# Performance work log

Hardware: AMD Instinct MI355X
Metric: run time of the kernel (lower is better)

## Reference

```python
import jax, jax.numpy as jnp
import numpy as np

B, H, N, D = 4, 8, 4096, 64
M = 266  # nb_features = int(D * ln(D))
CHUNK = 128
KERNEL_EPS = 1e-4


def _gaussian_orthogonal_random_matrix(nb_rows, nb_cols, rng):
    # scaling == 0: rows are orthogonal blocks rescaled by norms of iid gaussian rows
    blocks = []
    n_full = nb_rows // nb_cols
    for _ in range(n_full):
        q, _ = np.linalg.qr(rng.standard_normal((nb_cols, nb_cols)))
        blocks.append(q.T)
    rem = nb_rows - n_full * nb_cols
    if rem > 0:
        q, _ = np.linalg.qr(rng.standard_normal((nb_cols, nb_cols)))
        blocks.append(q.T[:rem])
    final = np.concatenate(blocks, axis=0)
    multiplier = np.linalg.norm(rng.standard_normal((nb_rows, nb_cols)), axis=1)
    return (multiplier[:, None] * final).astype(np.float32)


def setup_inputs() -> dict:
    key = jax.random.key(0)
    kq, kk, kv = jax.random.split(key, 3)
    rng = np.random.default_rng(0)
    return {
        "q": jax.random.normal(kq, (B, H, N, D), dtype=jnp.float32),
        "k": jax.random.normal(kk, (B, H, N, D), dtype=jnp.float32),
        "v": jax.random.normal(kv, (B, H, N, D), dtype=jnp.float32),
        "projection_matrix": jnp.asarray(
            _gaussian_orthogonal_random_matrix(M, D, rng)),
    }


def _softmax_kernel(data, projection_matrix, is_query):
    # data: [b,h,n,d], projection: [m,d]
    d = data.shape[-1]
    data_normalizer = d ** (-0.25)
    ratio = projection_matrix.shape[0] ** (-0.5)
    data_dash = jnp.einsum('bhnd,md->bhnm', data_normalizer * data,
                           projection_matrix)
    diag_data = jnp.sum(data ** 2, axis=-1) * 0.5 * data_normalizer ** 2  # [b,h,n]
    if is_query:
        stab = jnp.max(data_dash, axis=-1, keepdims=True)
    else:
        stab = jnp.max(data_dash)  # global max, as in torch reference
    return ratio * (jnp.exp(data_dash - diag_data[..., None] - stab) + KERNEL_EPS)


def _causal_linear_attention(qp, kp, v, chunk=CHUNK):
    # qp,kp: [b,h,n,m]; v: [b,h,n,e]; chunked causal cumulative-sum scan
    b, h, n, m = qp.shape
    e = v.shape[-1]
    nc = n // chunk
    qc = qp.reshape(b, h, nc, chunk, m).transpose(2, 0, 1, 3, 4)
    kc = kp.reshape(b, h, nc, chunk, m).transpose(2, 0, 1, 3, 4)
    vc = v.reshape(b, h, nc, chunk, e).transpose(2, 0, 1, 3, 4)

    def step(carry, inp):
        k_sum, ctx_sum = carry  # [b,h,m], [b,h,m,e]
        qch, kch, vch = inp     # [b,h,c,m], [b,h,c,m], [b,h,c,e]
        k_cs = k_sum[:, :, None, :] + jnp.cumsum(kch, axis=2)  # [b,h,c,m]
        D_inv = 1.0 / jnp.einsum('bhcm,bhcm->bhc', qch, k_cs)
        ctx = ctx_sum[:, :, None] + jnp.cumsum(
            jnp.einsum('bhcm,bhce->bhcme', kch, vch), axis=2)  # [b,h,c,m,e]
        out = jnp.einsum('bhcme,bhcm,bhc->bhce', ctx, qch, D_inv)
        return (k_cs[:, :, -1], ctx[:, :, -1]), out

    init = (jnp.zeros((b, h, m), qp.dtype), jnp.zeros((b, h, m, e), qp.dtype))
    _, outs = jax.lax.scan(step, init, (qc, kc, vc))
    return outs.transpose(1, 2, 0, 3, 4).reshape(b, h, n, e)


def reference(q, k, v, projection_matrix):
    qp = _softmax_kernel(q, projection_matrix, is_query=True)
    kp = _softmax_kernel(k, projection_matrix, is_query=False)
    return _causal_linear_attention(qp, kp, v)
```

## Files before the change

### kernel.cpp

```cpp
#include <hip/hip_runtime.h>

#define BB 4
#define HH 8
#define NSEQ 4096
#define DD 64
#define MM 266
#define CCH 128
#define NCH 32
#define NBH (BB*HH)
#define NROWS (NBH*NSEQ)

#define NORMALIZER 0.35355339059327373f
#define DIAGF 0.0625f
#define RATIO 0.0613140017f
#define KEPS 1e-4f
#define SBIAS 4.0f

typedef unsigned short ushort_t;
typedef unsigned int uint_t;

typedef __attribute__((ext_vector_type(8))) short bf16x8;
typedef __attribute__((ext_vector_type(4))) float f32x4;

__device__ __forceinline__ f32x4 mfma16(bf16x8 a, bf16x8 b, f32x4 c){
  return __builtin_amdgcn_mfma_f32_16x16x32_bf16(a, b, c, 0, 0, 0);
}

__device__ __forceinline__ ushort_t f2bf(float x){
  union { float f; uint_t u; } v; v.f = x;
  uint_t r = (v.u + 0x7FFFu + ((v.u >> 16) & 1u)) >> 16;
  return (ushort_t)r;
}
__device__ __forceinline__ float bf2f(ushort_t h){
  union { uint_t u; float f; } v; v.u = ((uint_t)h) << 16;
  return v.f;
}
__device__ __forceinline__ void unpack2(uint_t w, float& lo, float& hi){
  union { uint_t u; float f; } a, b;
  a.u = w << 16; b.u = w & 0xFFFF0000u;
  lo = a.f; hi = b.f;
}

__device__ __forceinline__ uint_t fenc(float f){
  uint_t b = __float_as_uint(f);
  return (b & 0x80000000u) ? ~b : (b | 0x80000000u);
}
__device__ __forceinline__ float fdec(uint_t u){
  uint_t b = (u >> 31) ? (u ^ 0x80000000u) : ~u;
  return __uint_as_float(b);
}

__device__ __forceinline__ bf16x8 frag_ld(const ushort_t* tile, int stride, int s0, int koff){
  const int l = threadIdx.x & 63;
  return *(const bf16x8*)(tile + (s0 + (l&15))*stride + koff + ((l>>4)<<3));
}


__global__ __launch_bounds__(256) void k_dash_both(const float* __restrict__ q,
                                                   const float* __restrict__ k,
                                                   const float* __restrict__ proj,
                                                   ushort_t* __restrict__ qp,
                                                   ushort_t* __restrict__ kd,
                                                   uint_t* __restrict__ gmaxu){
  __shared__ __align__(16) ushort_t pjs[272*72];
  __shared__ __align__(16) ushort_t qs[128*72];
  __shared__ float diags[128];
  __shared__ float smax[4];
  const int t = threadIdx.x;
  const bool isq = blockIdx.x < (NROWS/128);
  const int blk = isq ? blockIdx.x : (blockIdx.x - NROWS/128);
  const float* x = isq ? q : k;

  #pragma unroll
  for (int h=0; h<2; ++h){
    float2 pv[17];
    #pragma unroll
    for (int i=0;i<17;++i){
      int idx = t + (h*17+i)*256;
      int m = idx>>5, dp = (idx&31)*2;
      float2 p2 = {0.f,0.f};
      if (m < MM) p2 = *(const float2*)(proj + (size_t)m*DD + dp);
      pv[i] = p2;
    }
    #pragma unroll
    for (int i=0;i<17;++i){
      int idx = t + (h*17+i)*256;
      int m = idx>>5, dp = (idx&31)*2;
      *(uint_t*)(pjs + m*72 + dp) = (uint_t)f2bf(pv[i].x) | ((uint_t)f2bf(pv[i].y)<<16);
    }
  }
  {
    const int row = t>>1, half = t&1;
    const float2* xr = (const float2*)(x + ((size_t)blk*128 + row)*DD + half*32);
    float ss = 0.f;
    #pragma unroll
    for (int i=0;i<16;++i){
      float2 a = xr[i];
      ss += a.x*a.x + a.y*a.y;
      uint_t w = (uint_t)f2bf(a.x*NORMALIZER) | ((uint_t)f2bf(a.y*NORMALIZER)<<16);
      *(uint_t*)(qs + row*72 + half*32 + i*2) = w;
    }
    ss += __shfl_xor(ss, 1);
    if (half==0) diags[row] = ss*DIAGF;
  }
  __syncthreads();

  const int l = t&63, wv = t>>6;
  const int wr0 = wv*32;
  float dv[2][4];
  #pragma unroll
  for (int rt=0;rt<2;++rt)
    #pragma unroll
    for (int r=0;r<4;++r) dv[rt][r] = diags[wr0 + rt*16 + ((l>>4)<<2) + r];

  const size_t growb = (size_t)blk*128;

  if (isq){
    float rmax[2][4];
    #pragma unroll
    for (int rt=0;rt<2;++rt){ rmax[rt][0]=-3e38f; rmax[rt][1]=-3e38f; rmax[rt][2]=-3e38f; rmax[rt][3]=-3e38f; }
    uint_t spu[17][2][2];
    #pragma unroll
    for (int mt=0; mt<17; ++mt){
      bf16x8 b0 = frag_ld(pjs, 72, mt*16, 0);
      bf16x8 b1 = frag_ld(pjs, 72, mt*16, 32);
      const bool valid = (mt*16 + (l&15)) < MM;
      #pragma unroll
      for (int rt=0;rt<2;++rt){
        bf16x8 a0 = frag_ld(qs, 72, wr0+rt*16, 0);
        bf16x8 a1 = frag_ld(qs, 72, wr0+rt*16, 32);
        f32x4 acc = {0.f,0.f,0.f,0.f};
        acc = mfma16(a0, b0, acc);
        acc = mfma16(a1, b1, acc);
        float sp0 = acc[0]-dv[rt][0]+SBIAS, sp1 = acc[1]-dv[rt][1]+SBIAS;
        float sp2 = acc[2]-dv[rt][2]+SBIAS, sp3 = acc[3]-dv[rt][3]+SBIAS;
        if (valid){
          rmax[rt][0] = fmaxf(rmax[rt][0], sp0); rmax[rt][1] = fmaxf(rmax[rt][1], sp1);
          rmax[rt][2] = fmaxf(rmax[rt][2], sp2); rmax[rt][3] = fmaxf(rmax[rt][3], sp3);
        }
        spu[mt][rt][0] = (uint_t)f2bf(sp0) | ((uint_t)f2bf(sp1)<<16);
        spu[mt][rt][1] = (uint_t)f2bf(sp2) | ((uint_t)f2bf(sp3)<<16);
      }
    }
    float sub[2][4];
    #pragma unroll
    for (int rt=0;rt<2;++rt){
      #pragma unroll
      for (int r=0;r<4;++r){
        float m = rmax[rt][r];
        m = fmaxf(m, __shfl_xor(m,1)); m = fmaxf(m, __shfl_xor(m,2));
        m = fmaxf(m, __shfl_xor(m,4)); m = fmaxf(m, __shfl_xor(m,8));
        sub[rt][r] = m + dv[rt][r];
      }
    }
    #pragma unroll
    for (int mt=0; mt<17; ++mt){
      const int m = mt*16 + (l&15);
      if (m < MM){
        #pragma unroll
        for (int rt=0;rt<2;++rt){
          float a0,a1,a2,a3;
          unpack2(spu[mt][rt][0], a0, a1);
          unpack2(spu[mt][rt][1], a2, a3);
          const size_t rb = growb + wr0 + rt*16 + ((l>>4)<<2);
          qp[(rb+0)*MM + m] = f2bf(RATIO*(__expf(a0 - sub[rt][0]) + KEPS));
          qp[(rb+1)*MM + m] = f2bf(RATIO*(__expf(a1 - sub[rt][1]) + KEPS));
          qp[(rb+2)*MM + m] = f2bf(RATIO*(__expf(a2 - sub[rt][2]) + KEPS));
          qp[(rb+3)*MM + m] = f2bf(RATIO*(__expf(a3 - sub[rt][3]) + KEPS));
        }
      }
    }
  } else {
    float rmax[2][4];
    #pragma unroll
    for (int rt=0;rt<2;++rt){ rmax[rt][0]=-3e38f; rmax[rt][1]=-3e38f; rmax[rt][2]=-3e38f; rmax[rt][3]=-3e38f; }
    for (int mt=0; mt<17; ++mt){
      bf16x8 b0 = frag_ld(pjs, 72, mt*16, 0);
      bf16x8 b1 = frag_ld(pjs, 72, mt*16, 32);
      const int m = mt*16 + (l&15);
      const bool valid = (m < MM);
      #pragma unroll
      for (int rt=0;rt<2;++rt){
        bf16x8 a0 = frag_ld(qs, 72, wr0+rt*16, 0);
        bf16x8 a1 = frag_ld(qs, 72, wr0+rt*16, 32);
        f32x4 acc = {0.f,0.f,0.f,0.f};
        acc = mfma16(a0, b0, acc);
        acc = mfma16(a1, b1, acc);
        #pragma unroll
        for (int r=0;r<4;++r){
          float sp = acc[r] - dv[rt][r] + SBIAS;
          if (valid){
            rmax[rt][r] = fmaxf(rmax[rt][r], sp);
            kd[(growb + wr0 + rt*16 + ((l>>4)<<2) + r)*MM + m] = f2bf(sp);
          }
        }
      }
    }
    float bm = -3e38f;
    #pragma unroll
    for (int rt=0;rt<2;++rt){
      #pragma unroll
      for (int r=0;r<4;++r){
        float m = rmax[rt][r];
        m = fmaxf(m, __shfl_xor(m,1)); m = fmaxf(m, __shfl_xor(m,2));
        m = fmaxf(m, __shfl_xor(m,4)); m = fmaxf(m, __shfl_xor(m,8));
        bm = fmaxf(bm, m + dv[rt][r]);
      }
    }
    bm = fmaxf(bm, __shfl_xor(bm,16));
    bm = fmaxf(bm, __shfl_xor(bm,32));
    if (l==0) smax[wv] = bm;
    __syncthreads();
    if (t==0){
      float g = fmaxf(fmaxf(smax[0],smax[1]), fmaxf(smax[2],smax[3]));
      atomicMax(gmaxu, fenc(g));
    }
  }
}


__global__ __launch_bounds__(256) void k_chunksum8(const ushort_t* __restrict__ kd,
                                                   const float* __restrict__ v,
                                                   const uint_t* __restrict__ gmaxu,
                                                   ushort_t* __restrict__ ctx,
                                                   float* __restrict__ z){
  __shared__ __align__(16) ushort_t kpT[272*34];
  __shared__ __align__(16) ushort_t vT[64*136];
  const int blk = blockIdx.x, bh = blk>>5, ch = blk&31;
  const int t = threadIdx.x, l = t&63, wv = t>>6;
  const int row0 = ch*CCH;
  const ushort_t* kg = kd + (size_t)(bh*NSEQ + row0)*MM;
  const float*    vg = v  + (size_t)(bh*NSEQ + row0)*DD;
  const float g = fdec(gmaxu[0]);

  {
    const int e = t&63, rp = t>>6;
    float rv[32];
    #pragma unroll
    for (int i=0;i<16;++i){
      rv[2*i]   = vg[(size_t)(2*(rp+4*i)  )*DD + e];
      rv[2*i+1] = vg[(size_t)(2*(rp+4*i)+1)*DD + e];
    }
    #pragma unroll
    for (int i=0;i<16;++i)
      *(uint_t*)(vT + e*136 + 2*(rp+4*i)) =
        (uint_t)f2bf(rv[2*i]) | ((uint_t)f2bf(rv[2*i+1])<<16);
  }
  for (int idx=t; idx<6*34; idx+=256) kpT[266*34 + idx] = 0;

  const int rloc  = t>>3;
  const int mlane = t&7;
  const bool hastail = (mlane < 5);
  uint_t rw[17];

#define CLOAD(KS) do{ \
    const ushort_t* src_ = kg + (size_t)((KS)*32 + rloc)*MM; \
    _Pragma("unroll") \
    for (int j=0;j<16;++j) rw[j] = *(const uint_t*)(src_ + 2*(j*8 + mlane)); \
    rw[16] = hastail ? *(const uint_t*)(src_ + 2*(128 + mlane)) : 0u; \
  }while(0)

#define EXPPACK() do{ \
    _Pragma("unroll") \
    for (int j=0;j<17;++j){ \
      if (j < 16 || hastail){ \
        float a_, b_; unpack2(rw[j], a_, b_); \
        a_ = RATIO*(__expf(a_ - g) + KEPS); \
        b_ = RATIO*(__expf(b_ - g) + KEPS); \
        rw[j] = (uint_t)f2bf(a_) | ((uint_t)f2bf(b_)<<16); \
      } \
    } \
  }while(0)

#define CSTORE() do{ \
    _Pragma("unroll") \
    for (int j=0;j<16;++j){ \
      const int m_ = 2*(j*8 + mlane); \
      kpT[(m_  )*34 + rloc] = (ushort_t)rw[j]; \
      kpT[(m_+1)*34 + rloc] = (ushort_t)(rw[j]>>16); \
    } \
    if (hastail){ \
      const int m_ = 2*(128 + mlane); \
      kpT[(m_  )*34 + rloc] = (ushort_t)rw[16]; \
      kpT[(m_+1)*34 + rloc] = (ushort_t)(rw[16]>>16); \
    } \
  }while(0)

  f32x4 acc[17];
  #pragma unroll
  for (int i=0;i<17;++i) acc[i] = (f32x4){0.f,0.f,0.f,0.f};
  float zacc = 0.f, zacc2 = 0.f;
  const bool hasz2 = (256 + t) < MM;

  CLOAD(0);
  EXPPACK();
  for (int ks=0; ks<4; ++ks){
    __syncthreads();
    CSTORE();
    __syncthreads();
    if (ks < 3) CLOAD(ks+1);

    {
      float s1 = 0.f;
      #pragma unroll
      for (int j=0;j<16;++j){
        float a_, b_; unpack2(*(const uint_t*)(kpT + t*34 + 2*j), a_, b_);
        s1 += a_; s1 += b_;
      }
      zacc += s1;
      if (t < 16){
        float s2 = 0.f;
        #pragma unroll
        for (int j=0;j<16;++j){
          float a_, b_; unpack2(*(const uint_t*)(kpT + (256+t)*34 + 2*j), a_, b_);
          s2 += a_; s2 += b_;
        }
        zacc2 += s2;
      }
    }
    bf16x8 bv = frag_ld(vT, 136, wv*16, ks*32);
    #pragma unroll
    for (int mt=0; mt<17; ++mt){
      bf16x8 a = frag_ld(kpT, 34, mt*16, 0);
      acc[mt] = mfma16(a, bv, acc[mt]);
    }
    if (ks < 3) EXPPACK();
  }

  ushort_t* cg = ctx + (size_t)blk*MM*DD;
  const int e = wv*16 + (l&15);
  #pragma unroll
  for (int mt=0; mt<17; ++mt){
    #pragma unroll
    for (int r=0;r<4;++r){
      int m = mt*16 + ((l>>4)<<2) + r;
      if (m < MM) cg[(size_t)m*DD + e] = f2bf(acc[mt][r]);
    }
  }
  float* zgo = z + (size_t)blk*MM;
  zgo[t] = zacc;
  if (hasz2) zgo[256+t] = zacc2;
#undef CLOAD
#undef EXPPACK
#undef CSTORE
}


__global__ __launch_bounds__(256) void k_prefix3(ushort_t* __restrict__ ctx,
                                                 float* __restrict__ z){
  int bid = blockIdx.x;
  if (bid < NBH*67){
    int bh = bid/67, mg = bid%67;
    int t = threadIdx.x; int mo = t>>6, e = t&63;
    int m = mg*4 + mo;
    if (m >= MM) return;
    size_t base = (size_t)bh*NCH*MM*DD + (size_t)m*DD + e;
    float vals[32];
    #pragma unroll
    for (int c=0;c<NCH;++c) vals[c] = bf2f(ctx[base + (size_t)c*MM*DD]);
    float run = 0.f;
    #pragma unroll
    for (int c=0;c<NCH;++c){
      float cur = vals[c];
      ctx[base + (size_t)c*MM*DD] = f2bf(run);
      run += cur;
    }
  } else {
    int bh = bid - NBH*67, t = threadIdx.x;
    size_t base = (size_t)bh*NCH*MM;
    {
      float va[32];
      #pragma unroll
      for (int c=0;c<NCH;++c) va[c] = z[base + (size_t)c*MM + t];
      float run = 0.f;
      #pragma unroll
      for (int c=0;c<NCH;++c){ float cur = va[c]; z[base + (size_t)c*MM + t] = run; run += cur; }
    }
    if (256 + t < MM){
      float vb[32];
      #pragma unroll
      for (int c=0;c<NCH;++c) vb[c] = z[base + (size_t)c*MM + 256 + t];
      float run = 0.f;
      #pragma unroll
      for (int c=0;c<NCH;++c){ float cur = vb[c]; z[base + (size_t)c*MM + 256 + t] = run; run += cur; }
    }
  }
}


__global__ __launch_bounds__(512) void k_output11(const ushort_t* __restrict__ qp,
                                                  const ushort_t* __restrict__ kd,
                                                  const float* __restrict__ v,
                                                  const ushort_t* __restrict__ ctx,
                                                  const float* __restrict__ z,
                                                  const uint_t* __restrict__ gmaxu,
                                                  float* __restrict__ out){
  __shared__ __align__(16) char lds[52224];
  ushort_t* qs   = (ushort_t*)lds;
  ushort_t* kss  = (ushort_t*)(lds + 18432);
  ushort_t* Ps   = (ushort_t*)lds;
  ushort_t* ctxT = (ushort_t*)(lds + 36864);
  ushort_t* vT   = (ushort_t*)(lds + 34816);

  const int blk = blockIdx.x, bh = blk>>5, ch = blk&31;
  const int t = threadIdx.x, l = t&63, wv = t>>6;
  const int row0 = ch*CCH;
  const int wr0 = wv*16;
  const float g = fdec(gmaxu[0]);

  const ushort_t* qg = qp + (size_t)(bh*NSEQ + row0)*MM;
  const ushort_t* kg = kd + (size_t)(bh*NSEQ + row0)*MM;
  const float*    vg = v  + (size_t)(bh*NSEQ + row0)*DD;
  const ushort_t* ctxg = ctx + (size_t)blk*MM*DD;
  const float*    zg = z  + (size_t)blk*MM;

  const int mcol  = (t&31)<<1;
  const int qrow0 = t>>5;
  const int ce    = t&63;
  const int cm0   = t>>6;
  uint_t rq[8], rk[8];
  ushort_t rc[8];
  float rz;

#define LOADREGS(MT) do{ \
    const int m0_ = (MT)*64; \
    const bool vq_ = (m0_ + mcol) < MM; \
    _Pragma("unroll") \
    for (int i=0;i<8;++i){ \
      int row_ = qrow0 + 16*i; \
      rq[i] = vq_ ? *(const uint_t*)(qg + (size_t)row_*MM + m0_ + mcol) : 0u; \
      rk[i] = vq_ ? *(const uint_t*)(kg + (size_t)row_*MM + m0_ + mcol) : 0u; \
    } \
    _Pragma("unroll") \
    for (int i=0;i<8;++i){ \
      int mm_ = cm0 + 8*i; \
      rc[i] = (m0_ + mm_ < MM) ? ctxg[(size_t)(m0_ + mm_)*DD + ce] : (ushort_t)0; \
    } \
    rz = (m0_ + (t&63) < MM) ? zg[m0_ + (t&63)] : 0.f; \
  }while(0)

#define EXPPACKK(MT) do{ \
    const bool vq_ = ((MT)*64 + mcol) < MM; \
    if (vq_){ \
      _Pragma("unroll") \
      for (int i=0;i<8;++i){ \
        float a_, b_; unpack2(rk[i], a_, b_); \
        a_ = RATIO*(__expf(a_ - g) + KEPS); \
        b_ = RATIO*(__expf(b_ - g) + KEPS); \
        rk[i] = (uint_t)f2bf(a_) | ((uint_t)f2bf(b_)<<16); \
      } \
    } \
  }while(0)

#define WRITELDS() do{ \
    _Pragma("unroll") \
    for (int i=0;i<8;++i){ \
      int row_ = qrow0 + 16*i; \
      *(uint_t*)(qs + row_*72 + mcol) = rq[i]; \
      *(uint_t*)(kss + row_*72 + mcol) = rk[i]; \
    } \
    _Pragma("unroll") \
    for (int i=0;i<8;++i) ctxT[ce*72 + cm0 + 8*i] = rc[i]; \
    if (t < 64) ctxT[64*72 + t] = f2bf(rz); \
  }while(0)

  for (int idx=t; idx<15*72; idx+=512) ctxT[65*72 + idx] = 0;

  f32x4 acc[8];
  f32x4 oacc[5];
  #pragma unroll
  for (int ct=0;ct<8;++ct) acc[ct] = (f32x4){0.f,0.f,0.f,0.f};
  #pragma unroll
  for (int et=0;et<5;++et) oacc[et] = (f32x4){0.f,0.f,0.f,0.f};

  LOADREGS(0);
  EXPPACKK(0);
  for (int mt=0; mt<5; ++mt){
    __syncthreads();
    WRITELDS();
    __syncthreads();
    if (mt < 4) LOADREGS(mt+1);

    bf16x8 aq[2];
    aq[0] = frag_ld(qs, 72, wr0, 0);
    aq[1] = frag_ld(qs, 72, wr0, 32);
    #pragma unroll
    for (int ct=0;ct<8;++ct){
      bf16x8 b0 = frag_ld(kss, 72, ct*16, 0);
      bf16x8 b1 = frag_ld(kss, 72, ct*16, 32);
      acc[ct] = mfma16(aq[0], b0, acc[ct]);
      acc[ct] = mfma16(aq[1], b1, acc[ct]);
    }
    #pragma unroll
    for (int et=0;et<5;++et){
      bf16x8 b0 = frag_ld(ctxT, 72, et*16, 0);
      bf16x8 b1 = frag_ld(ctxT, 72, et*16, 32);
      oacc[et] = mfma16(aq[0], b0, oacc[et]);
      oacc[et] = mfma16(aq[1], b1, oacc[et]);
    }
    if (mt < 4) EXPPACKK(mt+1);
  }
  __syncthreads();

  float rv[16];
  const int rp = t>>6;
  {
    #pragma unroll
    for (int i=0;i<8;++i){
      rv[2*i]   = vg[(size_t)(2*(rp+8*i)  )*DD + ce];
      rv[2*i+1] = vg[(size_t)(2*(rp+8*i)+1)*DD + ce];
    }
  }

  float ds[4] = {0.f,0.f,0.f,0.f};
  #pragma unroll
  for (int ct=0;ct<8;++ct){
    #pragma unroll
    for (int r=0;r<4;++r){
      int i = wr0 + ((l>>4)<<2) + r;
      int j = ct*16 + (l&15);
      float m = (j <= i) ? acc[ct][r] : 0.f;
      acc[ct][r] = m;
      ds[r] += m;
    }
  }
  #pragma unroll
  for (int ct=0;ct<8;++ct){
    #pragma unroll
    for (int r=0;r<4;++r){
      int i = wr0 + ((l>>4)<<2) + r;
      Ps[i*136 + ct*16 + (l&15)] = f2bf(acc[ct][r]);
    }
  }
  float dtot[4];
  #pragma unroll
  for (int r=0;r<4;++r){
    float d = ds[r];
    d += __shfl_xor(d,1); d += __shfl_xor(d,2); d += __shfl_xor(d,4); d += __shfl_xor(d,8);
    dtot[r] = d + __shfl(oacc[4][r], l & 48);
  }
  {
    #pragma unroll
    for (int i=0;i<8;++i)
      *(uint_t*)(vT + ce*136 + 2*(rp+8*i)) =
        (uint_t)f2bf(rv[2*i]) | ((uint_t)f2bf(rv[2*i+1])<<16);
  }
  __syncthreads();

  #pragma unroll
  for (int kt=0;kt<4;++kt){
    bf16x8 ap = frag_ld(Ps, 136, wr0, kt*32);
    #pragma unroll
    for (int et=0;et<4;++et){
      bf16x8 bv = frag_ld(vT, 136, et*16, kt*32);
      oacc[et] = mfma16(ap, bv, oacc[et]);
    }
  }

  float* og = out + (size_t)(bh*NSEQ + row0)*DD;
  #pragma unroll
  for (int r=0;r<4;++r){
    int i = wr0 + ((l>>4)<<2) + r;
    float dinv = 1.0f / dtot[r];
    #pragma unroll
    for (int et=0;et<4;++et)
      og[(size_t)i*DD + et*16 + (l&15)] = oacc[et][r] * dinv;
  }
#undef LOADREGS
#undef EXPPACKK
#undef WRITELDS
}


extern "C" void kernel_launch(void* const* d_in, const int* in_sizes, int n_in,
                              void* d_out, int out_size, void* d_ws, size_t ws_size,
                              hipStream_t stream) {
  const float* q    = (const float*)d_in[0];
  const float* k    = (const float*)d_in[1];
  const float* v    = (const float*)d_in[2];
  const float* proj = (const float*)d_in[3];
  float* out = (float*)d_out;
  char* ws = (char*)d_ws;

  const size_t QP_OFF   = 0;
  const size_t KD_OFF   = 69730304ull;
  const size_t CTX_OFF  = 139460608ull;
  const size_t Z_OFF    = 174325760ull;
  const size_t GMAX_OFF = 175415296ull;
  if (ws_size < 175416000ull) return;

  ushort_t* qp   = (ushort_t*)(ws + QP_OFF);
  ushort_t* kd   = (ushort_t*)(ws + KD_OFF);
  ushort_t* ctx  = (ushort_t*)(ws + CTX_OFF);
  float* z       = (float*)(ws + Z_OFF);
  uint_t* gmaxu  = (uint_t*)(ws + GMAX_OFF);

  hipMemsetAsync(gmaxu, 0, 4, stream);
  k_dash_both<<<2*(NROWS/128), 256, 0, stream>>>(q, k, proj, qp, kd, gmaxu);
  k_chunksum8<<<NBH*NCH, 256, 0, stream>>>(kd, v, gmaxu, ctx, z);
  k_prefix3  <<<NBH*67 + NBH, 256, 0, stream>>>(ctx, z);
  k_output11 <<<NBH*NCH, 512, 0, stream>>>(qp, kd, v, ctx, z, gmaxu, out);
}
```

Baseline: 198.9 us.

## Stream projection matrix through small LDS tile in dash kernel

The dash kernel no longer stages the whole 266x64 projection matrix in shared memory. It loads it in five 64-row slices, prefetching the next slice into registers while the current one is multiplied. Shared memory per block drops from about 57 KB to about 28 KB, so more blocks can be resident per CU. In exchange the kernel adds extra barriers, and both branches now keep register-resident spu arrays and a prefetch buffer, which raises register pressure.

```diff
diff --git a/kernel.cpp b/kernel.cpp
--- a/kernel.cpp
+++ b/kernel.cpp
@@ -56,13 +56,13 @@
 }
 
 
-__global__ __launch_bounds__(256) void k_dash_both(const float* __restrict__ q,
-                                                   const float* __restrict__ k,
-                                                   const float* __restrict__ proj,
-                                                   ushort_t* __restrict__ qp,
-                                                   ushort_t* __restrict__ kd,
-                                                   uint_t* __restrict__ gmaxu){
-  __shared__ __align__(16) ushort_t pjs[272*72];
+__global__ __launch_bounds__(256) void k_dash_both3(const float* __restrict__ q,
+                                                    const float* __restrict__ k,
+                                                    const float* __restrict__ proj,
+                                                    ushort_t* __restrict__ qp,
+                                                    ushort_t* __restrict__ kd,
+                                                    uint_t* __restrict__ gmaxu){
+  __shared__ __align__(16) ushort_t pj[64*72];
   __shared__ __align__(16) ushort_t qs[128*72];
   __shared__ float diags[128];
   __shared__ float smax[4];
@@ -71,24 +71,6 @@
   const int blk = isq ? blockIdx.x : (blockIdx.x - NROWS/128);
   const float* x = isq ? q : k;
 
-  #pragma unroll
-  for (int h=0; h<2; ++h){
-    float2 pv[17];
-    #pragma unroll
-    for (int i=0;i<17;++i){
-      int idx = t + (h*17+i)*256;
-      int m = idx>>5, dp = (idx&31)*2;
-      float2 p2 = {0.f,0.f};
-      if (m < MM) p2 = *(const float2*)(proj + (size_t)m*DD + dp);
-      pv[i] = p2;
-    }
-    #pragma unroll
-    for (int i=0;i<17;++i){
-      int idx = t + (h*17+i)*256;
-      int m = idx>>5, dp = (idx&31)*2;
-      *(uint_t*)(pjs + m*72 + dp) = (uint_t)f2bf(pv[i].x) | ((uint_t)f2bf(pv[i].y)<<16);
-    }
-  }
   {
     const int row = t>>1, half = t&1;
     const float2* xr = (const float2*)(x + ((size_t)blk*128 + row)*DD + half*32);
@@ -115,33 +97,83 @@
 
   const size_t growb = (size_t)blk*128;
 
+  uint_t pw[9];
+#define PLOAD(MT5) do{ \
+    _Pragma("unroll") \
+    for (int j=0;j<9;++j){ \
+      int idx = t + j*256; \
+      int row_ = idx/36, cu_ = idx - row_*36; \
+      int m_ = (MT5)*64 + row_; \
+      uint_t w_ = 0; \
+      if (m_ < MM){ \
+        float2 p2_ = *(const float2*)(proj + (size_t)m_*DD + cu_*2); \
+        w_ = (uint_t)f2bf(p2_.x) | ((uint_t)f2bf(p2_.y)<<16); \
+      } \
+      pw[j] = w_; \
+    } \
+  }while(0)
+#define PWRITE() do{ \
+    _Pragma("unroll") \
+    for (int j=0;j<9;++j){ \
+      int idx = t + j*256; \
+      int row_ = idx/36, cu_ = idx - row_*36; \
+      *(uint_t*)(pj + row_*72 + cu_*2) = pw[j]; \
+    } \
+  }while(0)
+
+  float rmax[2][4];
+  #pragma unroll
+  for (int rt=0;rt<2;++rt){ rmax[rt][0]=-3e38f; rmax[rt][1]=-3e38f; rmax[rt][2]=-3e38f; rmax[rt][3]=-3e38f; }
+  uint_t spu[17][2][2];
+
+  PLOAD(0);
+  #pragma unroll
+  for (int mt5=0; mt5<5; ++mt5){
+    __syncthreads();
+    PWRITE();
+    __syncthreads();
+    if (mt5 < 4) PLOAD(mt5+1);
+
+    #pragma unroll
+    for (int sub=0; sub<4; ++sub){
+      const int mt = mt5*4 + sub;
+      if (mt < 17){
+        bf16x8 b0 = frag_ld(pj, 72, sub*16, 0);
+        bf16x8 b1 = frag_ld(pj, 72, sub*16, 32);
+        const int m = mt*16 + (l&15);
+        const bool valid = (m < MM);
+        #pragma unroll
+        for (int rt=0;rt<2;++rt){
+          bf16x8 a0 = frag_ld(qs, 72, wr0+rt*16, 0);
+          bf16x8 a1 = frag_ld(qs, 72, wr0+rt*16, 32);
+          f32x4 acc = {0.f,0.f,0.f,0.f};
+          acc = mfma16(a0, b0, acc);
+          acc = mfma16(a1, b1, acc);
+          if (isq){
+            float sp0 = acc[0]-dv[rt][0]+SBIAS, sp1 = acc[1]-dv[rt][1]+SBIAS;
+            float sp2 = acc[2]-dv[rt][2]+SBIAS, sp3 = acc[3]-dv[rt][3]+SBIAS;
+            if (valid){
+              rmax[rt][0] = fmaxf(rmax[rt][0], sp0); rmax[rt][1] = fmaxf(rmax[rt][1], sp1);
+              rmax[rt][2] = fmaxf(rmax[rt][2], sp2); rmax[rt][3] = fmaxf(rmax[rt][3], sp3);
+            }
+            spu[mt][rt][0] = (uint_t)f2bf(sp0) | ((uint_t)f2bf(sp1)<<16);
+            spu[mt][rt][1] = (uint_t)f2bf(sp2) | ((uint_t)f2bf(sp3)<<16);
+          } else {
+            #pragma unroll
+            for (int r=0;r<4;++r){
+              float sp = acc[r] - dv[rt][r] + SBIAS;
+              if (valid){
+                rmax[rt][r] = fmaxf(rmax[rt][r], sp);
+                kd[(growb + wr0 + rt*16 + ((l>>4)<<2) + r)*MM + m] = f2bf(sp);
+              }
+            }
+          }
+        }
+      }
+    }
+  }
+
   if (isq){
-    float rmax[2][4];
-    #pragma unroll
-    for (int rt=0;rt<2;++rt){ rmax[rt][0]=-3e38f; rmax[rt][1]=-3e38f; rmax[rt][2]=-3e38f; rmax[rt][3]=-3e38f; }
-    uint_t spu[17][2][2];
-    #pragma unroll
-    for (int mt=0; mt<17; ++mt){
-      bf16x8 b0 = frag_ld(pjs, 72, mt*16, 0);
-      bf16x8 b1 = frag_ld(pjs, 72, mt*16, 32);
-      const bool valid = (mt*16 + (l&15)) < MM;
-      #pragma unroll
-      for (int rt=0;rt<2;++rt){
-        bf16x8 a0 = frag_ld(qs, 72, wr0+rt*16, 0);
-        bf16x8 a1 = frag_ld(qs, 72, wr0+rt*16, 32);
-        f32x4 acc = {0.f,0.f,0.f,0.f};
-        acc = mfma16(a0, b0, acc);
-        acc = mfma16(a1, b1, acc);
-        float sp0 = acc[0]-dv[rt][0]+SBIAS, sp1 = acc[1]-dv[rt][1]+SBIAS;
-        float sp2 = acc[2]-dv[rt][2]+SBIAS, sp3 = acc[3]-dv[rt][3]+SBIAS;
-        if (valid){
-          rmax[rt][0] = fmaxf(rmax[rt][0], sp0); rmax[rt][1] = fmaxf(rmax[rt][1], sp1);
-          rmax[rt][2] = fmaxf(rmax[rt][2], sp2); rmax[rt][3] = fmaxf(rmax[rt][3], sp3);
-        }
-        spu[mt][rt][0] = (uint_t)f2bf(sp0) | ((uint_t)f2bf(sp1)<<16);
-        spu[mt][rt][1] = (uint_t)f2bf(sp2) | ((uint_t)f2bf(sp3)<<16);
-      }
-    }
     float sub[2][4];
     #pragma unroll
     for (int rt=0;rt<2;++rt){
@@ -171,31 +203,6 @@
       }
     }
   } else {
-    float rmax[2][4];
-    #pragma unroll
-    for (int rt=0;rt<2;++rt){ rmax[rt][0]=-3e38f; rmax[rt][1]=-3e38f; rmax[rt][2]=-3e38f; rmax[rt][3]=-3e38f; }
-    for (int mt=0; mt<17; ++mt){
-      bf16x8 b0 = frag_ld(pjs, 72, mt*16, 0);
-      bf16x8 b1 = frag_ld(pjs, 72, mt*16, 32);
-      const int m = mt*16 + (l&15);
-      const bool valid = (m < MM);
-      #pragma unroll
-      for (int rt=0;rt<2;++rt){
-        bf16x8 a0 = frag_ld(qs, 72, wr0+rt*16, 0);
-        bf16x8 a1 = frag_ld(qs, 72, wr0+rt*16, 32);
-        f32x4 acc = {0.f,0.f,0.f,0.f};
-        acc = mfma16(a0, b0, acc);
-        acc = mfma16(a1, b1, acc);
-        #pragma unroll
-        for (int r=0;r<4;++r){
-          float sp = acc[r] - dv[rt][r] + SBIAS;
-          if (valid){
-            rmax[rt][r] = fmaxf(rmax[rt][r], sp);
-            kd[(growb + wr0 + rt*16 + ((l>>4)<<2) + r)*MM + m] = f2bf(sp);
-          }
-        }
-      }
-    }
     float bm = -3e38f;
     #pragma unroll
     for (int rt=0;rt<2;++rt){
@@ -216,6 +223,8 @@
       atomicMax(gmaxu, fenc(g));
     }
   }
+#undef PLOAD
+#undef PWRITE
 }
 
 
@@ -596,8 +605,8 @@
   uint_t* gmaxu  = (uint_t*)(ws + GMAX_OFF);
 
   hipMemsetAsync(gmaxu, 0, 4, stream);
-  k_dash_both<<<2*(NROWS/128), 256, 0, stream>>>(q, k, proj, qp, kd, gmaxu);
-  k_chunksum8<<<NBH*NCH, 256, 0, stream>>>(kd, v, gmaxu, ctx, z);
-  k_prefix3  <<<NBH*67 + NBH, 256, 0, stream>>>(ctx, z);
-  k_output11 <<<NBH*NCH, 512, 0, stream>>>(qp, kd, v, ctx, z, gmaxu, out);
-}
+  k_dash_both3<<<2*(NROWS/128), 256, 0, stream>>>(q, k, proj, qp, kd, gmaxu);
+  k_chunksum8 <<<NBH*NCH, 256, 0, stream>>>(kd, v, gmaxu, ctx, z);
+  k_prefix3   <<<NBH*67 + NBH, 256, 0, stream>>>(ctx, z);
+  k_output11  <<<NBH*NCH, 512, 0, stream>>>(qp, kd, v, ctx, z, gmaxu, out);
+}
```

New measurement: 199.8 us. No clear change (+0.4%).
